# Optimization experiments

Measured on AMD Instinct MI355X. Metric: run time of the kernel, lower is better.

## Reference

```python
import jax, jax.numpy as jnp
import numpy as np

E = 8
HID = 2048
INTER = 1408
TOT = 8192


def setup_inputs() -> dict:
    key = jax.random.key(0)
    k1, k2, k3, k4, k5 = jax.random.split(key, 5)
    # uneven token counts per expert that sum exactly to TOT (grouped-GEMM ragged sizes)
    deltas = np.array([512, -256, 128, -384, 256, -512, 384, -128], dtype=np.int32)
    tokens_per_expert = jnp.asarray(TOT // E + deltas, dtype=jnp.int32)  # sums to TOT
    permuted_x = jax.random.normal(k1, (TOT, HID), dtype=jnp.float32)
    permuted_probs = jax.random.uniform(k2, (TOT,), dtype=jnp.float32)
    s_in = 1.0 / np.sqrt(HID)
    s_mid = 1.0 / np.sqrt(INTER)
    w_gate = jax.random.normal(k3, (E, HID, INTER), dtype=jnp.float32) * s_in
    w_up = jax.random.normal(k4, (E, HID, INTER), dtype=jnp.float32) * s_in
    w_down = jax.random.normal(k5, (E, INTER, HID), dtype=jnp.float32) * s_mid
    return {
        "permuted_x": permuted_x,
        "permuted_probs": permuted_probs,
        "w_gate": w_gate,
        "w_up": w_up,
        "w_down": w_down,
        "tokens_per_expert": tokens_per_expert,
    }


def reference(permuted_x, permuted_probs, w_gate, w_up, w_down, tokens_per_expert):
    # Grouped GEMM: tokens sorted by expert; lax.ragged_dot contracts each
    # contiguous group of rows against its expert's weight without padding.
    gate = jax.lax.ragged_dot(permuted_x, w_gate, tokens_per_expert)  # [T, INTER]
    up = jax.lax.ragged_dot(permuted_x, w_up, tokens_per_expert)      # [T, INTER]
    h = jax.nn.silu(gate) * up                                         # fused SiLU-mul
    values = jax.lax.ragged_dot(h, w_down, tokens_per_expert)          # [T, HID]
    return permuted_probs[:, None].astype(values.dtype) * values
```

## Files before the change

kernel.cpp:

```cpp
#include <hip/hip_runtime.h>

typedef unsigned short u16;
typedef unsigned int u32;
typedef u16 us8 __attribute__((ext_vector_type(8)));
typedef __bf16 bf16x8 __attribute__((ext_vector_type(8)));
typedef float f32x4 __attribute__((ext_vector_type(4)));

constexpr int kE = 8;
constexpr int kHID = 2048;
constexpr int kINTER = 1408;
constexpr int kTOT = 8192;

static __device__ __forceinline__ u16 f2bf(float f) {
  u32 u = __float_as_uint(f);
  u32 r = (u + 0x7fffu + ((u >> 16) & 1u)) >> 16;
  return (u16)r;
}

static __device__ __forceinline__ void gll16(const u16* g, u16* l) {
  __builtin_amdgcn_global_load_lds(
      (const __attribute__((address_space(1))) u32*)g,
      (__attribute__((address_space(3))) u32*)l, 16, 0, 0);
}

__global__ void conv_bf16(const float* __restrict__ x, u16* __restrict__ o) {
  size_t i = ((size_t)blockIdx.x * 256 + threadIdx.x) * 8;
  const float4* p = (const float4*)(x + i);
  float4 f0 = p[0], f1 = p[1];
  us8 v;
  v[0] = f2bf(f0.x); v[1] = f2bf(f0.y); v[2] = f2bf(f0.z); v[3] = f2bf(f0.w);
  v[4] = f2bf(f1.x); v[5] = f2bf(f1.y); v[6] = f2bf(f1.z); v[7] = f2bf(f1.w);
  *(us8*)(o + i) = v;
}

__global__ void transp_bf16(const float* __restrict__ w, u16* __restrict__ wt,
                            int K, int N) {
  __shared__ float tile[64][65];
  int e = blockIdx.z;
  const float* we = w + (size_t)e * K * N;
  u16* wte = wt + (size_t)e * K * N;
  int n0 = blockIdx.x * 64, k0 = blockIdx.y * 64;
  int t = threadIdx.x;
  int kl = t >> 4, n4 = (t & 15) * 4;
#pragma unroll
  for (int r = 0; r < 4; r++) {
    int k = r * 16 + kl;
    float4 v = *(const float4*)(we + (size_t)(k0 + k) * N + n0 + n4);
    tile[k][n4 + 0] = v.x; tile[k][n4 + 1] = v.y;
    tile[k][n4 + 2] = v.z; tile[k][n4 + 3] = v.w;
  }
  __syncthreads();
#pragma unroll
  for (int r = 0; r < 2; r++) {
    int c = r * 256 + t;
    int n = c >> 3, kc = (c & 7) * 8;
    us8 o;
#pragma unroll
    for (int j = 0; j < 8; j++) o[j] = f2bf(tile[kc + j][n]);
    *(us8*)(wte + (size_t)(n0 + n) * K + k0 + kc) = o;
  }
}

__global__ void transp_gu(const float* __restrict__ wgp, const float* __restrict__ wup,
                          u16* __restrict__ Wgt, u16* __restrict__ Wut) {
  __shared__ float tile[64][65];
  int z = blockIdx.z;
  int e = z & 7;
  const float* w = (z < kE) ? wgp : wup;
  u16* wt = (z < kE) ? Wgt : Wut;
  const int K = kHID, N = kINTER;
  const float* we = w + (size_t)e * K * N;
  u16* wte = wt + (size_t)e * K * N;
  int n0 = blockIdx.x * 64, k0 = blockIdx.y * 64;
  int t = threadIdx.x;
  int kl = t >> 4, n4 = (t & 15) * 4;
#pragma unroll
  for (int r = 0; r < 4; r++) {
    int k = r * 16 + kl;
    float4 v = *(const float4*)(we + (size_t)(k0 + k) * N + n0 + n4);
    tile[k][n4 + 0] = v.x; tile[k][n4 + 1] = v.y;
    tile[k][n4 + 2] = v.z; tile[k][n4 + 3] = v.w;
  }
  __syncthreads();
#pragma unroll
  for (int r = 0; r < 2; r++) {
    int c = r * 256 + t;
    int n = c >> 3, kc = (c & 7) * 8;
    us8 o;
#pragma unroll
    for (int j = 0; j < 8; j++) o[j] = f2bf(tile[kc + j][n]);
    *(us8*)(wte + (size_t)(n0 + n) * K + k0 + kc) = o;
  }
}

static __device__ __forceinline__ bool expert_of_tile256(
    const int* __restrict__ tpe, int ty, int& e, int& m0, int& m_end) {
  int tile_base = 0, row_base = 0;
  e = -1;
  for (int i = 0; i < kE; i++) {
    int tc = tpe[i];
    int nt = (tc + 255) >> 8;
    if (e < 0 && ty < tile_base + nt) {
      e = i;
      m0 = row_base + (ty - tile_base) * 256;
      m_end = row_base + tc;
    }
    tile_base += nt;
    row_base += tc;
  }
  return e >= 0;
}

static __device__ __forceinline__ void map_block(int& bx, int& by) {
  int nx = gridDim.x, ny = gridDim.y;
  int nwg = nx * ny;
  int flat = blockIdx.y * nx + blockIdx.x;
  int q = nwg >> 3, r = nwg & 7;
  int xcd = flat & 7, lid = flat >> 3;
  int nf = (xcd < r ? xcd * (q + 1) : r * (q + 1) + (xcd - r) * q) + lid;
  const int G = 4;
  int gs = G * nx;
  int grp = nf / gs;
  int wi = nf - grp * gs;
  int rows = ny - grp * G;
  if (rows > G) rows = G;
  bx = wi / rows;
  by = grp * G + (wi - bx * rows);
}

__launch_bounds__(512, 2)
__global__ void gemm1(const u16* __restrict__ Xb, const u16* __restrict__ Wgt,
                      const u16* __restrict__ Wut, const float* __restrict__ probs,
                      const int* __restrict__ tpe, u16* __restrict__ H) {
  __shared__ __align__(16) u16 sm[65536];
  u16* A0 = sm;           u16* A1 = sm + 16384;
  u16* Bg0 = sm + 32768;  u16* Bg1 = sm + 40960;
  u16* Bu0 = sm + 49152;  u16* Bu1 = sm + 57344;

  int bx, by; map_block(bx, by);
  int e, m0, m_end;
  if (!expert_of_tile256(tpe, by, e, m0, m_end)) return;
  int n0 = bx * 128;

  int t = threadIdx.x;
  int w = t >> 6, lane = t & 63;
  int quad = lane >> 4, l15 = lane & 15;
  int wm = (w >> 1) * 64, wn = (w & 1) * 64;

  int trow = t >> 3;
  int cg = (t & 7) ^ (trow & 7);
  const u16* gA[4];
#pragma unroll
  for (int rr = 0; rr < 4; rr++) {
    int row = m0 + rr * 64 + trow;
    if (row > kTOT - 1) row = kTOT - 1;
    gA[rr] = Xb + (size_t)row * kHID + cg * 8;
  }
  const u16 *gBg[2], *gBu[2];
#pragma unroll
  for (int rr = 0; rr < 2; rr++) {
    size_t nrow = (size_t)e * kINTER + n0 + rr * 64 + trow;
    gBg[rr] = Wgt + nrow * kHID + cg * 8;
    gBu[rr] = Wut + nrow * kHID + cg * 8;
  }

  int abase = (wm + l15) * 64;
  int bbase = (wn + l15) * 64;
  int sz0 = ((quad ^ (l15 & 7)) << 3);
  int sz1 = (((4 | quad) ^ (l15 & 7)) << 3);

  f32x4 accg[4][4] = {};
  f32x4 accu[4][4] = {};

  auto stage = [&](u16* A, u16* Bg, u16* Bu, int ko) {
#pragma unroll
    for (int rr = 0; rr < 4; rr++) gll16(gA[rr] + ko, A + (rr * 64 + w * 8) * 64);
#pragma unroll
    for (int rr = 0; rr < 2; rr++) {
      gll16(gBg[rr] + ko, Bg + (rr * 64 + w * 8) * 64);
      gll16(gBu[rr] + ko, Bu + (rr * 64 + w * 8) * 64);
    }
  };
  auto compute = [&](const u16* A, const u16* Bg, const u16* Bu) {
#pragma unroll
    for (int ks = 0; ks < 2; ks++) {
      int sz = ks ? sz1 : sz0;
      bf16x8 a[4], bg[4], bu[4];
#pragma unroll
      for (int i = 0; i < 4; i++) a[i] = *(const bf16x8*)(A + abase + i * 1024 + sz);
#pragma unroll
      for (int j = 0; j < 4; j++) {
        bg[j] = *(const bf16x8*)(Bg + bbase + j * 1024 + sz);
        bu[j] = *(const bf16x8*)(Bu + bbase + j * 1024 + sz);
      }
#pragma unroll
      for (int i = 0; i < 4; i++)
#pragma unroll
        for (int j = 0; j < 4; j++) {
          accg[i][j] = __builtin_amdgcn_mfma_f32_16x16x32_bf16(a[i], bg[j], accg[i][j], 0, 0, 0);
          accu[i][j] = __builtin_amdgcn_mfma_f32_16x16x32_bf16(a[i], bu[j], accu[i][j], 0, 0, 0);
        }
    }
  };

  stage(A0, Bg0, Bu0, 0);
  __syncthreads();
  for (int kt = 0; kt < kHID / 64; kt += 2) {
    stage(A1, Bg1, Bu1, (kt + 1) * 64);
    compute(A0, Bg0, Bu0);
    __syncthreads();
    if (kt + 2 < kHID / 64) stage(A0, Bg0, Bu0, (kt + 2) * 64);
    compute(A1, Bg1, Bu1);
    __syncthreads();
  }

#pragma unroll
  for (int i = 0; i < 4; i++) {
#pragma unroll
    for (int r = 0; r < 4; r++) {
      int row = m0 + wm + i * 16 + quad * 4 + r;
      if (row < m_end) {
        float p = probs[row];
#pragma unroll
        for (int j = 0; j < 4; j++) {
          int col = n0 + wn + j * 16 + l15;
          float g = accg[i][j][r], u = accu[i][j][r];
          float s = g / (1.0f + __expf(-g));
          H[(size_t)row * kINTER + col] = f2bf(s * u * p);
        }
      }
    }
  }
}

__launch_bounds__(512, 2)
__global__ void gemm2(const u16* __restrict__ H, const u16* __restrict__ Wdt,
                      const int* __restrict__ tpe, float* __restrict__ out) {
  __shared__ __align__(16) u16 sm[49152];
  u16* A0 = sm;          u16* A1 = sm + 16384;
  u16* B0 = sm + 32768;  u16* B1 = sm + 40960;

  int bx, by; map_block(bx, by);
  int e, m0, m_end;
  if (!expert_of_tile256(tpe, by, e, m0, m_end)) return;
  int n0 = bx * 128;

  int t = threadIdx.x;
  int w = t >> 6, lane = t & 63;
  int quad = lane >> 4, l15 = lane & 15;
  int wm = (w >> 1) * 64, wn = (w & 1) * 64;

  int trow = t >> 3;
  int cg = (t & 7) ^ (trow & 7);
  const u16* gA[4];
#pragma unroll
  for (int rr = 0; rr < 4; rr++) {
    int row = m0 + rr * 64 + trow;
    if (row > kTOT - 1) row = kTOT - 1;
    gA[rr] = H + (size_t)row * kINTER + cg * 8;
  }
  const u16* gB[2];
#pragma unroll
  for (int rr = 0; rr < 2; rr++) {
    size_t nrow = (size_t)e * kHID + n0 + rr * 64 + trow;
    gB[rr] = Wdt + nrow * kINTER + cg * 8;
  }

  int abase = (wm + l15) * 64;
  int bbase = (wn + l15) * 64;
  int sz0 = ((quad ^ (l15 & 7)) << 3);
  int sz1 = (((4 | quad) ^ (l15 & 7)) << 3);

  f32x4 acc[4][4] = {};

  auto stage = [&](u16* A, u16* B, int ko) {
#pragma unroll
    for (int rr = 0; rr < 4; rr++) gll16(gA[rr] + ko, A + (rr * 64 + w * 8) * 64);
#pragma unroll
    for (int rr = 0; rr < 2; rr++) gll16(gB[rr] + ko, B + (rr * 64 + w * 8) * 64);
  };
  auto compute = [&](const u16* A, const u16* B) {
#pragma unroll
    for (int ks = 0; ks < 2; ks++) {
      int sz = ks ? sz1 : sz0;
      bf16x8 a[4], b[4];
#pragma unroll
      for (int i = 0; i < 4; i++) a[i] = *(const bf16x8*)(A + abase + i * 1024 + sz);
#pragma unroll
      for (int j = 0; j < 4; j++) b[j] = *(const bf16x8*)(B + bbase + j * 1024 + sz);
#pragma unroll
      for (int i = 0; i < 4; i++)
#pragma unroll
        for (int j = 0; j < 4; j++)
          acc[i][j] = __builtin_amdgcn_mfma_f32_16x16x32_bf16(a[i], b[j], acc[i][j], 0, 0, 0);
    }
  };

  stage(A0, B0, 0);
  __syncthreads();
  for (int kt = 0; kt < kINTER / 64; kt += 2) {
    stage(A1, B1, (kt + 1) * 64);
    compute(A0, B0);
    __syncthreads();
    if (kt + 2 < kINTER / 64) stage(A0, B0, (kt + 2) * 64);
    compute(A1, B1);
    __syncthreads();
  }

#pragma unroll
  for (int i = 0; i < 4; i++) {
#pragma unroll
    for (int r = 0; r < 4; r++) {
      int row = m0 + wm + i * 16 + quad * 4 + r;
      if (row < m_end) {
#pragma unroll
        for (int j = 0; j < 4; j++) {
          int col = n0 + wn + j * 16 + l15;
          out[(size_t)row * kHID + col] = acc[i][j][r];
        }
      }
    }
  }
}

extern "C" void kernel_launch(void* const* d_in, const int* in_sizes, int n_in,
                              void* d_out, int out_size, void* d_ws, size_t ws_size,
                              hipStream_t stream) {
  const float* x = (const float*)d_in[0];
  const float* probs = (const float*)d_in[1];
  const float* wg = (const float*)d_in[2];
  const float* wu = (const float*)d_in[3];
  const float* wd = (const float*)d_in[4];
  const int* tpe = (const int*)d_in[5];
  float* out = (float*)d_out;

  u16* ws = (u16*)d_ws;
  u16* Xb = ws;
  u16* Wgt = Xb + (size_t)kTOT * kHID;
  u16* Wut = Wgt + (size_t)kE * kINTER * kHID;
  u16* Wdt = Wut + (size_t)kE * kINTER * kHID;
  u16* H = Wdt + (size_t)kE * kHID * kINTER;

  conv_bf16<<<(kTOT * kHID) / (256 * 8), 256, 0, stream>>>(x, Xb);
  transp_gu<<<dim3(kINTER / 64, kHID / 64, 2 * kE), 256, 0, stream>>>(wg, wu, Wgt, Wut);
  transp_bf16<<<dim3(kHID / 64, kINTER / 64, kE), 256, 0, stream>>>(wd, Wdt, kINTER, kHID);

  gemm1<<<dim3(kINTER / 128, 39), 512, 0, stream>>>(Xb, Wgt, Wut, probs, tpe, H);
  gemm2<<<dim3(kHID / 128, 39), 512, 0, stream>>>(H, Wdt, tpe, out);
}
```

Measured before the change: 538.2 us.

## Shrink grouped GEMM tiles to 128x128 with K=32 stages for occupancy

Both grouped GEMMs move from 256x128 tiles with K=64 stages to 128x128 tiles with K=32 stages. Each of the 8 waves now covers 64x32 instead of 64x64, and the LDS swizzle is rebuilt for 32-wide rows. Smaller LDS footprint and launch bounds of 4 aim at more resident blocks and less ragged-tail padding, with 72 M-tiles instead of 39. The cost is lower arithmetic intensity per block, more global traffic for weight re-reads, and twice as many barriers per K.

```diff
diff --git a/kernel.cpp b/kernel.cpp
--- a/kernel.cpp
+++ b/kernel.cpp
@@ -93,16 +93,16 @@
   }
 }
 
-static __device__ __forceinline__ bool expert_of_tile256(
+static __device__ __forceinline__ bool expert_of_tile(
     const int* __restrict__ tpe, int ty, int& e, int& m0, int& m_end) {
   int tile_base = 0, row_base = 0;
   e = -1;
   for (int i = 0; i < kE; i++) {
     int tc = tpe[i];
-    int nt = (tc + 255) >> 8;
+    int nt = (tc + 127) >> 7;
     if (e < 0 && ty < tile_base + nt) {
       e = i;
-      m0 = row_base + (ty - tile_base) * 256;
+      m0 = row_base + (ty - tile_base) * 128;
       m_end = row_base + tc;
     }
     tile_base += nt;
@@ -128,89 +128,76 @@
   by = grp * G + (wi - bx * rows);
 }
 
-__launch_bounds__(512, 2)
+__launch_bounds__(512, 4)
 __global__ void gemm1(const u16* __restrict__ Xb, const u16* __restrict__ Wgt,
                       const u16* __restrict__ Wut, const float* __restrict__ probs,
                       const int* __restrict__ tpe, u16* __restrict__ H) {
-  __shared__ __align__(16) u16 sm[65536];
-  u16* A0 = sm;           u16* A1 = sm + 16384;
-  u16* Bg0 = sm + 32768;  u16* Bg1 = sm + 40960;
-  u16* Bu0 = sm + 49152;  u16* Bu1 = sm + 57344;
+  __shared__ __align__(16) u16 sm[24576];
 
   int bx, by; map_block(bx, by);
   int e, m0, m_end;
-  if (!expert_of_tile256(tpe, by, e, m0, m_end)) return;
+  if (!expert_of_tile(tpe, by, e, m0, m_end)) return;
   int n0 = bx * 128;
 
   int t = threadIdx.x;
   int w = t >> 6, lane = t & 63;
   int quad = lane >> 4, l15 = lane & 15;
-  int wm = (w >> 1) * 64, wn = (w & 1) * 64;
-
-  int trow = t >> 3;
-  int cg = (t & 7) ^ (trow & 7);
-  const u16* gA[4];
-#pragma unroll
-  for (int rr = 0; rr < 4; rr++) {
-    int row = m0 + rr * 64 + trow;
-    if (row > kTOT - 1) row = kTOT - 1;
-    gA[rr] = Xb + (size_t)row * kHID + cg * 8;
-  }
-  const u16 *gBg[2], *gBu[2];
-#pragma unroll
-  for (int rr = 0; rr < 2; rr++) {
-    size_t nrow = (size_t)e * kINTER + n0 + rr * 64 + trow;
-    gBg[rr] = Wgt + nrow * kHID + cg * 8;
-    gBu[rr] = Wut + nrow * kHID + cg * 8;
-  }
-
-  int abase = (wm + l15) * 64;
-  int bbase = (wn + l15) * 64;
-  int sz0 = ((quad ^ (l15 & 7)) << 3);
-  int sz1 = (((4 | quad) ^ (l15 & 7)) << 3);
-
-  f32x4 accg[4][4] = {};
-  f32x4 accu[4][4] = {};
-
-  auto stage = [&](u16* A, u16* Bg, u16* Bu, int ko) {
-#pragma unroll
-    for (int rr = 0; rr < 4; rr++) gll16(gA[rr] + ko, A + (rr * 64 + w * 8) * 64);
-#pragma unroll
-    for (int rr = 0; rr < 2; rr++) {
-      gll16(gBg[rr] + ko, Bg + (rr * 64 + w * 8) * 64);
-      gll16(gBu[rr] + ko, Bu + (rr * 64 + w * 8) * 64);
+  int wm = (w >> 2) * 64, wn = (w & 3) * 32;
+
+  int trow = t >> 2;
+  int cg = (t & 3) ^ ((t >> 3) & 3);
+  int arow = m0 + trow; if (arow > kTOT - 1) arow = kTOT - 1;
+  const u16* gA = Xb + (size_t)arow * kHID + cg * 8;
+  size_t nrow = (size_t)e * kINTER + n0 + trow;
+  const u16* gBg = Wgt + nrow * kHID + cg * 8;
+  const u16* gBu = Wut + nrow * kHID + cg * 8;
+  u16* dst = sm + w * 512;
+
+  int cs = ((l15 >> 1) & 3);
+  int sz = ((quad ^ cs) << 3);
+  int aoff[4], boff[2];
+#pragma unroll
+  for (int i = 0; i < 4; i++) aoff[i] = (wm + i * 16 + l15) * 32 + sz;
+#pragma unroll
+  for (int j = 0; j < 2; j++) boff[j] = (wn + j * 16 + l15) * 32 + sz;
+
+  f32x4 accg[4][2] = {};
+  f32x4 accu[4][2] = {};
+
+  auto stage = [&](int buf, int ko) {
+    u16* d = dst + buf * 12288;
+    gll16(gA + ko, d);
+    gll16(gBg + ko, d + 4096);
+    gll16(gBu + ko, d + 8192);
+  };
+  auto compute = [&](int buf) {
+    const u16* b = sm + buf * 12288;
+    bf16x8 a[4], bg[2], bu[2];
+#pragma unroll
+    for (int i = 0; i < 4; i++) a[i] = *(const bf16x8*)(b + aoff[i]);
+#pragma unroll
+    for (int j = 0; j < 2; j++) {
+      bg[j] = *(const bf16x8*)(b + 4096 + boff[j]);
+      bu[j] = *(const bf16x8*)(b + 8192 + boff[j]);
     }
+#pragma unroll
+    for (int i = 0; i < 4; i++)
+#pragma unroll
+      for (int j = 0; j < 2; j++) {
+        accg[i][j] = __builtin_amdgcn_mfma_f32_16x16x32_bf16(a[i], bg[j], accg[i][j], 0, 0, 0);
+        accu[i][j] = __builtin_amdgcn_mfma_f32_16x16x32_bf16(a[i], bu[j], accu[i][j], 0, 0, 0);
+      }
   };
-  auto compute = [&](const u16* A, const u16* Bg, const u16* Bu) {
-#pragma unroll
-    for (int ks = 0; ks < 2; ks++) {
-      int sz = ks ? sz1 : sz0;
-      bf16x8 a[4], bg[4], bu[4];
-#pragma unroll
-      for (int i = 0; i < 4; i++) a[i] = *(const bf16x8*)(A + abase + i * 1024 + sz);
-#pragma unroll
-      for (int j = 0; j < 4; j++) {
-        bg[j] = *(const bf16x8*)(Bg + bbase + j * 1024 + sz);
-        bu[j] = *(const bf16x8*)(Bu + bbase + j * 1024 + sz);
-      }
-#pragma unroll
-      for (int i = 0; i < 4; i++)
-#pragma unroll
-        for (int j = 0; j < 4; j++) {
-          accg[i][j] = __builtin_amdgcn_mfma_f32_16x16x32_bf16(a[i], bg[j], accg[i][j], 0, 0, 0);
-          accu[i][j] = __builtin_amdgcn_mfma_f32_16x16x32_bf16(a[i], bu[j], accu[i][j], 0, 0, 0);
-        }
-    }
-  };
-
-  stage(A0, Bg0, Bu0, 0);
+
+  constexpr int NK = kHID / 32;
+  stage(0, 0);
   __syncthreads();
-  for (int kt = 0; kt < kHID / 64; kt += 2) {
-    stage(A1, Bg1, Bu1, (kt + 1) * 64);
-    compute(A0, Bg0, Bu0);
+  for (int kt = 0; kt < NK; kt += 2) {
+    stage(1, (kt + 1) * 32);
+    compute(0);
     __syncthreads();
-    if (kt + 2 < kHID / 64) stage(A0, Bg0, Bu0, (kt + 2) * 64);
-    compute(A1, Bg1, Bu1);
+    if (kt + 2 < NK) stage(0, (kt + 2) * 32);
+    compute(1);
     __syncthreads();
   }
 
@@ -222,7 +209,7 @@
       if (row < m_end) {
         float p = probs[row];
 #pragma unroll
-        for (int j = 0; j < 4; j++) {
+        for (int j = 0; j < 2; j++) {
           int col = n0 + wn + j * 16 + l15;
           float g = accg[i][j][r], u = accu[i][j][r];
           float s = g / (1.0f + __expf(-g));
@@ -233,77 +220,67 @@
   }
 }
 
-__launch_bounds__(512, 2)
+__launch_bounds__(512, 4)
 __global__ void gemm2(const u16* __restrict__ H, const u16* __restrict__ Wdt,
                       const int* __restrict__ tpe, float* __restrict__ out) {
-  __shared__ __align__(16) u16 sm[49152];
-  u16* A0 = sm;          u16* A1 = sm + 16384;
-  u16* B0 = sm + 32768;  u16* B1 = sm + 40960;
+  __shared__ __align__(16) u16 sm[16384];
 
   int bx, by; map_block(bx, by);
   int e, m0, m_end;
-  if (!expert_of_tile256(tpe, by, e, m0, m_end)) return;
+  if (!expert_of_tile(tpe, by, e, m0, m_end)) return;
   int n0 = bx * 128;
 
   int t = threadIdx.x;
   int w = t >> 6, lane = t & 63;
   int quad = lane >> 4, l15 = lane & 15;
-  int wm = (w >> 1) * 64, wn = (w & 1) * 64;
-
-  int trow = t >> 3;
-  int cg = (t & 7) ^ (trow & 7);
-  const u16* gA[4];
-#pragma unroll
-  for (int rr = 0; rr < 4; rr++) {
-    int row = m0 + rr * 64 + trow;
-    if (row > kTOT - 1) row = kTOT - 1;
-    gA[rr] = H + (size_t)row * kINTER + cg * 8;
-  }
-  const u16* gB[2];
-#pragma unroll
-  for (int rr = 0; rr < 2; rr++) {
-    size_t nrow = (size_t)e * kHID + n0 + rr * 64 + trow;
-    gB[rr] = Wdt + nrow * kINTER + cg * 8;
-  }
-
-  int abase = (wm + l15) * 64;
-  int bbase = (wn + l15) * 64;
-  int sz0 = ((quad ^ (l15 & 7)) << 3);
-  int sz1 = (((4 | quad) ^ (l15 & 7)) << 3);
-
-  f32x4 acc[4][4] = {};
-
-  auto stage = [&](u16* A, u16* B, int ko) {
-#pragma unroll
-    for (int rr = 0; rr < 4; rr++) gll16(gA[rr] + ko, A + (rr * 64 + w * 8) * 64);
-#pragma unroll
-    for (int rr = 0; rr < 2; rr++) gll16(gB[rr] + ko, B + (rr * 64 + w * 8) * 64);
+  int wm = (w >> 2) * 64, wn = (w & 3) * 32;
+
+  int trow = t >> 2;
+  int cg = (t & 3) ^ ((t >> 3) & 3);
+  int arow = m0 + trow; if (arow > kTOT - 1) arow = kTOT - 1;
+  const u16* gA = H + (size_t)arow * kINTER + cg * 8;
+  size_t nrow = (size_t)e * kHID + n0 + trow;
+  const u16* gB = Wdt + nrow * kINTER + cg * 8;
+  u16* dst = sm + w * 512;
+
+  int cs = ((l15 >> 1) & 3);
+  int sz = ((quad ^ cs) << 3);
+  int aoff[4], boff[2];
+#pragma unroll
+  for (int i = 0; i < 4; i++) aoff[i] = (wm + i * 16 + l15) * 32 + sz;
+#pragma unroll
+  for (int j = 0; j < 2; j++) boff[j] = (wn + j * 16 + l15) * 32 + sz;
+
+  f32x4 acc[4][2] = {};
+
+  auto stage = [&](int buf, int ko) {
+    u16* d = dst + buf * 8192;
+    gll16(gA + ko, d);
+    gll16(gB + ko, d + 4096);
   };
-  auto compute = [&](const u16* A, const u16* B) {
-#pragma unroll
-    for (int ks = 0; ks < 2; ks++) {
-      int sz = ks ? sz1 : sz0;
-      bf16x8 a[4], b[4];
-#pragma unroll
-      for (int i = 0; i < 4; i++) a[i] = *(const bf16x8*)(A + abase + i * 1024 + sz);
-#pragma unroll
-      for (int j = 0; j < 4; j++) b[j] = *(const bf16x8*)(B + bbase + j * 1024 + sz);
-#pragma unroll
-      for (int i = 0; i < 4; i++)
-#pragma unroll
-        for (int j = 0; j < 4; j++)
-          acc[i][j] = __builtin_amdgcn_mfma_f32_16x16x32_bf16(a[i], b[j], acc[i][j], 0, 0, 0);
-    }
+  auto compute = [&](int buf) {
+    const u16* b = sm + buf * 8192;
+    bf16x8 a[4], bb[2];
+#pragma unroll
+    for (int i = 0; i < 4; i++) a[i] = *(const bf16x8*)(b + aoff[i]);
+#pragma unroll
+    for (int j = 0; j < 2; j++) bb[j] = *(const bf16x8*)(b + 4096 + boff[j]);
+#pragma unroll
+    for (int i = 0; i < 4; i++)
+#pragma unroll
+      for (int j = 0; j < 2; j++)
+        acc[i][j] = __builtin_amdgcn_mfma_f32_16x16x32_bf16(a[i], bb[j], acc[i][j], 0, 0, 0);
   };
 
-  stage(A0, B0, 0);
+  constexpr int NK = kINTER / 32;
+  stage(0, 0);
   __syncthreads();
-  for (int kt = 0; kt < kINTER / 64; kt += 2) {
-    stage(A1, B1, (kt + 1) * 64);
-    compute(A0, B0);
+  for (int kt = 0; kt < NK; kt += 2) {
+    stage(1, (kt + 1) * 32);
+    compute(0);
     __syncthreads();
-    if (kt + 2 < kINTER / 64) stage(A0, B0, (kt + 2) * 64);
-    compute(A1, B1);
+    if (kt + 2 < NK) stage(0, (kt + 2) * 32);
+    compute(1);
     __syncthreads();
   }
 
@@ -314,7 +291,7 @@
       int row = m0 + wm + i * 16 + quad * 4 + r;
       if (row < m_end) {
 #pragma unroll
-        for (int j = 0; j < 4; j++) {
+        for (int j = 0; j < 2; j++) {
           int col = n0 + wn + j * 16 + l15;
           out[(size_t)row * kHID + col] = acc[i][j][r];
         }
@@ -345,6 +322,6 @@
   transp_gu<<<dim3(kINTER / 64, kHID / 64, 2 * kE), 256, 0, stream>>>(wg, wu, Wgt, Wut);
   transp_bf16<<<dim3(kHID / 64, kINTER / 64, kE), 256, 0, stream>>>(wd, Wdt, kINTER, kHID);
 
-  gemm1<<<dim3(kINTER / 128, 39), 512, 0, stream>>>(Xb, Wgt, Wut, probs, tpe, H);
-  gemm2<<<dim3(kHID / 128, 39), 512, 0, stream>>>(H, Wdt, tpe, out);
-}
+  gemm1<<<dim3(kINTER / 128, 72), 512, 0, stream>>>(Xb, Wgt, Wut, probs, tpe, H);
+  gemm2<<<dim3(kHID / 128, 72), 512, 0, stream>>>(H, Wdt, tpe, out);
+}
```

Result: no change. 532.4 us (-1.1%).
